# Kernel tuning notes

Measured on AMD Instinct MI355X. Metric: run time of the kernel, lower is better.

The kernel has to match this reference:

```python
import jax, jax.numpy as jnp
import numpy as np

# Static config (matches init_kwargs)
H, G, D = 16, 4, 128          # n_head, n_query_groups, head_size
QPK = H // G                  # queries per kv group = 4
LEFT = 1024 - 1               # sliding-window left width (local_window-1)
SCALE = 1.0 / float(np.sqrt(D))
NEG = jnp.finfo(jnp.float32).min


def _rope(x, cos, sin):
    # x: [B,T,h,D]; cos/sin: [T, D/2]; non-interleaved (flash-attn) convention
    d2 = cos.shape[-1]
    x1, x2 = x[..., :d2], x[..., d2:]
    c = cos[None, :, None, :]
    s = sin[None, :, None, :]
    return jnp.concatenate([x1 * c - x2 * s, x1 * s + x2 * c], axis=-1)


def setup_inputs() -> dict:
    key = jax.random.key(0)
    ks = jax.random.split(key, 4)
    B, T, C = 1, 2048, 2048
    x = jax.random.normal(ks[0], (B, T, C), jnp.float32)
    # real RoPE tables, base 10000
    pos = jnp.arange(T, dtype=jnp.float32)
    inv_freq = 1.0 / (10000.0 ** (jnp.arange(0, D, 2, dtype=jnp.float32) / D))
    ang = pos[:, None] * inv_freq[None, :]        # [T, D/2]
    cos, sin = jnp.cos(ang), jnp.sin(ang)
    W_attn = jax.random.normal(ks[1], ((H + 2 * G) * D, C), jnp.float32) * 0.02
    W_proj = jax.random.normal(ks[2], (C, H * D), jnp.float32) * 0.02
    k_sink = jax.random.normal(ks[3], (G * D,), jnp.float32) * 0.02
    v_sink = jnp.zeros((G * D,), jnp.float32)     # buffer, zeros in original
    return {"x": x, "cos": cos, "sin": sin, "W_attn": W_attn,
            "W_proj": W_proj, "k_sink": k_sink, "v_sink": v_sink}


def reference(x, cos, sin, W_attn, W_proj, k_sink, v_sink):
    B, T, C = x.shape
    # fused QKV projection (no bias)
    qkv = jnp.einsum('btc,oc->bto', x, W_attn)                 # [B,T,(H+2G)*D]
    qkv = qkv.reshape(B, T, G, QPK + 2, D)
    q = qkv[:, :, :, :QPK, :].reshape(B, T, H, D)              # [B,T,H,D]
    k = qkv[:, :, :, QPK, :]                                   # [B,T,G,D]
    v = qkv[:, :, :, QPK + 1, :]                               # [B,T,G,D]
    # RoPE on q and k
    q = _rope(q, cos, sin)
    k = _rope(k, cos, sin)
    # prepend sink token to k/v -> seqlen_k = T+1
    k = jnp.concatenate([jnp.broadcast_to(k_sink.reshape(1, 1, G, D), (B, 1, G, D)), k], axis=1)
    v = jnp.concatenate([jnp.broadcast_to(v_sink.reshape(1, 1, G, D), (B, 1, G, D)), v], axis=1)
    Tk = T + 1
    # GQA: group-major query head layout -> head h uses kv group h // QPK
    kh = jnp.repeat(k, QPK, axis=2)                            # [B,Tk,H,D]
    vh = jnp.repeat(v, QPK, axis=2)
    scores = jnp.einsum('bqhd,bkhd->bhqk', q, kh) * SCALE      # [B,H,T,Tk]
    # flash-attn causal + sliding window, bottom-right aligned: offset = Tk - T
    off = Tk - T
    i = jnp.arange(T)[:, None]
    j = jnp.arange(Tk)[None, :]
    allowed = (j <= i + off) & (j >= i + off - LEFT)
    scores = jnp.where(allowed[None, None], scores, NEG)
    p = jax.nn.softmax(scores, axis=-1)
    o = jnp.einsum('bhqk,bkhd->bqhd', p, vh).reshape(B, T, H * D)
    y = jnp.einsum('btd,cd->btc', o, W_proj)                   # output proj, no bias
    return y
```

## Files before the change

kernel.cpp:

```cpp
#include <hip/hip_runtime.h>

#define T_SEQ  2048
#define TK_SEQ 2049
#define JP     2080
#define SL_F    0.12751744f
#define THR_L2  11.0f

typedef __attribute__((ext_vector_type(8))) short short8;
typedef __attribute__((ext_vector_type(4))) float f32x4;

__device__ __forceinline__ unsigned short f2bf(float f) {
  unsigned int u = __float_as_uint(f);
  u += 0x7fff + ((u >> 16) & 1);
  return (unsigned short)(u >> 16);
}

__device__ __forceinline__ void gload16(const unsigned short* g, unsigned short* l) {
  __builtin_amdgcn_global_load_lds(
      (const __attribute__((address_space(1))) void*)g,
      (__attribute__((address_space(3))) void*)l, 16, 0, 0);
}

__global__ __launch_bounds__(256) void split_pack(const float4* __restrict__ s0,
                                                  unsigned short* __restrict__ d0,
                                                  int n0, int p0,
                                                  const float4* __restrict__ s1,
                                                  unsigned short* __restrict__ d1,
                                                  int n1, int p1) {
  int i = blockIdx.x * 256 + threadIdx.x;
  const float4* s; unsigned short* d; int k, p;
  if (i < n0) { s = s0; d = d0; k = i; p = p0; }
  else { k = i - n0; if (k >= n1) return; s = s1; d = d1; p = p1; }
  float4 f = s[k];
  float fv[4] = {f.x, f.y, f.z, f.w};
  ushort4 hv, lv;
#pragma unroll
  for (int e = 0; e < 4; ++e) {
    unsigned int u = __float_as_uint(fv[e]) & 0xffff0000u;
    ((unsigned short*)&hv)[e] = (unsigned short)(u >> 16);
    ((unsigned short*)&lv)[e] = f2bf(fv[e] - __uint_as_float(u));
  }
  *(ushort4*)(d + 4 * (size_t)k)     = hv;
  *(ushort4*)(d + p + 4 * (size_t)k) = lv;
}

__global__ __launch_bounds__(256, 2) void gemm_sp(const unsigned short* __restrict__ Ag,
                                                  const unsigned short* __restrict__ Bg,
                                                  float* __restrict__ C,
                                                  int M, int N, int K) {
  __shared__ unsigned short Ah[2][128 * 32], Al[2][128 * 32];
  __shared__ unsigned short Bh[2][128 * 32], Bl[2][128 * 32];

  const int tid  = threadIdx.x;
  const int lane = tid & 63;
  const int wid  = tid >> 6;
  const int wm   = (wid >> 1) << 6;
  const int wn   = (wid & 1) << 6;
  const int lo16 = lane & 15;
  const int hi4  = lane >> 4;
  const int m0   = blockIdx.y << 7;
  const int n0   = blockIdx.x << 7;
  const size_t MK = (size_t)M * K;
  const size_t NK = (size_t)N * K;

  const int c0 = (wid << 6) + lane;
  const int c1 = ((4 + wid) << 6) + lane;
  const unsigned short* a0g = Ag + (size_t)(m0 + (c0 >> 2)) * K + ((c0 & 3) << 3);
  const unsigned short* a1g = Ag + (size_t)(m0 + (c1 >> 2)) * K + ((c1 & 3) << 3);
  const unsigned short* b0g = Bg + (size_t)(n0 + (c0 >> 2)) * K + ((c0 & 3) << 3);
  const unsigned short* b1g = Bg + (size_t)(n0 + (c1 >> 2)) * K + ((c1 & 3) << 3);
  const int o0 = wid << 9;
  const int o1 = (4 + wid) << 9;

  int ra[4], rb[4];
#pragma unroll
  for (int i = 0; i < 4; ++i) {
    ra[i] = ((wm + i * 16 + lo16) << 5) + (hi4 << 3);
    rb[i] = ((wn + i * 16 + lo16) << 5) + (hi4 << 3);
  }

  f32x4 acc[4][4];
  const f32x4 z4 = {0.f, 0.f, 0.f, 0.f};
#pragma unroll
  for (int i = 0; i < 4; ++i)
#pragma unroll
    for (int j = 0; j < 4; ++j) acc[i][j] = z4;

  gload16(a0g,      &Ah[0][o0]);
  gload16(a1g,      &Ah[0][o1]);
  gload16(a0g + MK, &Al[0][o0]);
  gload16(a1g + MK, &Al[0][o1]);
  gload16(b0g,      &Bh[0][o0]);
  gload16(b1g,      &Bh[0][o1]);
  gload16(b0g + NK, &Bl[0][o0]);
  gload16(b1g + NK, &Bl[0][o1]);

  int cur = 0;
  for (int k0 = 0; k0 < K; k0 += 32) {
    const bool more = (k0 + 32) < K;
    if (more) {
      const int nxt = cur ^ 1;
      const int kn  = k0 + 32;
      gload16(a0g + kn,      &Ah[nxt][o0]);
      gload16(a1g + kn,      &Ah[nxt][o1]);
      gload16(a0g + MK + kn, &Al[nxt][o0]);
      gload16(a1g + MK + kn, &Al[nxt][o1]);
      gload16(b0g + kn,      &Bh[nxt][o0]);
      gload16(b1g + kn,      &Bh[nxt][o1]);
      gload16(b0g + NK + kn, &Bl[nxt][o0]);
      gload16(b1g + NK + kn, &Bl[nxt][o1]);
      asm volatile("s_waitcnt vmcnt(8)" ::: "memory");
    } else {
      asm volatile("s_waitcnt vmcnt(0)" ::: "memory");
    }
    __builtin_amdgcn_s_barrier();
    __builtin_amdgcn_sched_barrier(0);

    short8 fah[4], fal[4], fbh[4], fbl[4];
#pragma unroll
    for (int i = 0; i < 4; ++i) {
      fah[i] = *(const short8*)&Ah[cur][ra[i]];
      fal[i] = *(const short8*)&Al[cur][ra[i]];
      fbh[i] = *(const short8*)&Bh[cur][rb[i]];
      fbl[i] = *(const short8*)&Bl[cur][rb[i]];
    }
#pragma unroll
    for (int i = 0; i < 4; ++i)
#pragma unroll
      for (int j = 0; j < 4; ++j) {
        acc[i][j] = __builtin_amdgcn_mfma_f32_16x16x32_bf16(fah[i], fbh[j], acc[i][j], 0, 0, 0);
        acc[i][j] = __builtin_amdgcn_mfma_f32_16x16x32_bf16(fal[i], fbh[j], acc[i][j], 0, 0, 0);
        acc[i][j] = __builtin_amdgcn_mfma_f32_16x16x32_bf16(fah[i], fbl[j], acc[i][j], 0, 0, 0);
      }

    __builtin_amdgcn_sched_barrier(0);
    __builtin_amdgcn_s_barrier();
    asm volatile("" ::: "memory");
    cur ^= 1;
  }

#pragma unroll
  for (int i = 0; i < 4; ++i) {
    const int row = m0 + wm + i * 16 + (hi4 << 2);
#pragma unroll
    for (int j = 0; j < 4; ++j) {
      float* cp = C + (size_t)row * N + n0 + wn + j * 16 + lo16;
      cp[0]            = acc[i][j][0];
      cp[(size_t)N]    = acc[i][j][1];
      cp[(size_t)2*N]  = acc[i][j][2];
      cp[(size_t)3*N]  = acc[i][j][3];
    }
  }
}

#define RB_Q  4096
#define RB_K  1024
#define RB_KE 64
#define RB_V  65

__global__ __launch_bounds__(256) void rope2(const float* __restrict__ qkv,
                                             const float* __restrict__ cosb,
                                             const float* __restrict__ sinb,
                                             const float* __restrict__ ksink,
                                             const float* __restrict__ vsink,
                                             unsigned short* __restrict__ qb,
                                             unsigned short* __restrict__ kb,
                                             unsigned short* __restrict__ vtb) {
  __shared__ unsigned short tl[512 * 33];
  const int bid = blockIdx.x, tid = threadIdx.x;
  if (bid < RB_Q) {
    int idx = bid * 256 + tid;
    int t = idx >> 9, rem = idx & 511;
    int h = rem >> 5, dp = (rem & 31) << 1;
    int g = h >> 2, qi = h & 3;
    const float* src = qkv + (size_t)t * 3072 + g * 768 + qi * 128;
    float2 x1 = *(const float2*)(src + dp);
    float2 x2 = *(const float2*)(src + 64 + dp);
    float2 c  = *(const float2*)(cosb + t * 64 + dp);
    float2 s  = *(const float2*)(sinb + t * 64 + dp);
    ushort2 o1 = { f2bf(x1.x * c.x - x2.x * s.x), f2bf(x1.y * c.y - x2.y * s.y) };
    ushort2 o2 = { f2bf(x1.x * s.x + x2.x * c.x), f2bf(x1.y * s.y + x2.y * c.y) };
    *(ushort2*)(qb + (size_t)t * 2048 + h * 128 + dp)      = o1;
    *(ushort2*)(qb + (size_t)t * 2048 + h * 128 + 64 + dp) = o2;
  } else if (bid < RB_Q + RB_K) {
    int idx = (bid - RB_Q) * 256 + tid;
    int t = idx >> 7, rem = idx & 127;
    int g = rem >> 5, dp = (rem & 31) << 1;
    const float* src = qkv + (size_t)t * 3072 + g * 768 + 512;
    float2 x1 = *(const float2*)(src + dp);
    float2 x2 = *(const float2*)(src + 64 + dp);
    float2 c  = *(const float2*)(cosb + t * 64 + dp);
    float2 s  = *(const float2*)(sinb + t * 64 + dp);
    ushort2 o1 = { f2bf(x1.x * c.x - x2.x * s.x), f2bf(x1.y * c.y - x2.y * s.y) };
    ushort2 o2 = { f2bf(x1.x * s.x + x2.x * c.x), f2bf(x1.y * s.y + x2.y * c.y) };
    size_t base = (size_t)(t + 1) * 512 + g * 128 + dp;
    *(ushort2*)(kb + base)      = o1;
    *(ushort2*)(kb + base + 64) = o2;
  } else if (bid < RB_Q + RB_K + RB_KE) {
    int idx = (bid - RB_Q - RB_K) * 256 + tid;
    int jj = idx >> 9, c = idx & 511;
    if (jj == 0) kb[c] = f2bf(ksink[c]);
    else         kb[(size_t)(2048 + jj) * 512 + c] = 0;
  } else {
    int b  = bid - RB_Q - RB_K - RB_KE;
    int j0 = b << 5;
#pragma unroll 4
    for (int st = 0; st < 64; ++st) {
      int id = st * 256 + tid;
      int jj = id >> 9, c = id & 511;
      int j = j0 + jj;
      float val;
      if (j == 0)          val = vsink[c];
      else if (j <= T_SEQ) val = qkv[(size_t)(j - 1) * 3072 + (c >> 7) * 768 + 640 + (c & 127)];
      else                 val = 0.f;
      tl[c * 33 + jj] = f2bf(val);
    }
    __syncthreads();
#pragma unroll 4
    for (int st = 0; st < 32; ++st) {
      int id = st * 256 + tid;
      int row = id >> 4, jp = (id & 15) << 1;
      ushort2 w = { tl[row * 33 + jp], tl[row * 33 + jp + 1] };
      *(ushort2*)(vtb + (size_t)row * JP + j0 + jp) = w;
    }
  }
}

#define KSTR 136
#define VSTR 40

__global__ __launch_bounds__(512) void attn_mfma_bf16(const unsigned short* __restrict__ qb,
                                                      const unsigned short* __restrict__ kb,
                                                      const unsigned short* __restrict__ vtb,
                                                      unsigned short* __restrict__ ofh,
                                                      const float4* __restrict__ wpsrc,
                                                      unsigned short* __restrict__ wps) {
  __shared__ unsigned short Kl[2][32 * KSTR];
  __shared__ unsigned short Vl[2][128 * VSTR];

  const int bid  = blockIdx.x;
  const int tid  = threadIdx.x;
  if (bid >= 256) {
    int k = (bid - 256) * 512 + tid;
    float4 f = wpsrc[k];
    float fv[4] = {f.x, f.y, f.z, f.w};
    ushort4 hv, lv;
#pragma unroll
    for (int e = 0; e < 4; ++e) {
      unsigned int u = __float_as_uint(fv[e]) & 0xffff0000u;
      ((unsigned short*)&hv)[e] = (unsigned short)(u >> 16);
      ((unsigned short*)&lv)[e] = f2bf(fv[e] - __uint_as_float(u));
    }
    *(ushort4*)(wps + 4 * (size_t)k)           = hv;
    *(ushort4*)(wps + 4194304 + 4 * (size_t)k) = lv;
    return;
  }

  const int tile = bid >> 2;
  const int g    = bid & 3;
  const int t0b  = tile << 5;
  const int wv   = tid >> 6;
  const int hq   = wv & 3;
  const int sub  = wv >> 2;
  const int h    = g * 4 + hq;
  const int lane = tid & 63;
  const int lo   = lane & 15;
  const int hi   = lane >> 4;
  const int t0w  = t0b + (sub << 4);
  const int t    = t0w + lo;

  const int sj   = tid >> 4;
  const int sc   = (tid & 15) << 3;
  const int kphi = ((((sj & 7) << 2) | (sj >> 3))) * KSTR + sc;
  const int svd  = tid >> 2;
  const int svj  = (tid & 3) << 3;
  const int vdst = svd * VSTR + svj;
  const unsigned short* ksrc = kb  + (size_t)sj * 512 + g * 128 + sc;
  const unsigned short* vsrc = vtb + (size_t)(g * 128 + svd) * JP + svj;

  short8 qfrag[4];
  {
    const unsigned short* qp = qb + (size_t)t * 2048 + h * 128 + (hi << 3);
#pragma unroll
    for (int d0 = 0; d0 < 4; ++d0) qfrag[d0] = *(const short8*)(qp + d0 * 32);
  }

  f32x4 acc[8];
  const f32x4 z4 = {0.f, 0.f, 0.f, 0.f};
#pragma unroll
  for (int dt = 0; dt < 8; ++dt) acc[dt] = z4;

  float m = -1e4f, l = 0.f;

  int jlo = t0b - 1022; if (jlo < 0) jlo = 0;
  const int jb0  = jlo & ~31;
  const int jmax = t0b + 32;
  const int nch  = ((jmax - jb0) >> 5) + 1;

  const int klA = (((lo & 3) << 2) | (lo >> 2)) * KSTR + (hi << 3);

  uint4 kreg = *(const uint4*)(ksrc + (size_t)jb0 * 512);
  uint4 vreg = *(const uint4*)(vsrc + jb0);
  *(uint4*)&Kl[0][kphi] = kreg;
  *(uint4*)&Vl[0][vdst] = vreg;
  __syncthreads();

  int bsel = 0;
  for (int ci = 0; ci < nch; ++ci) {
    const int jb = jb0 + (ci << 5);
    const bool more = (ci + 1 < nch);
    if (more) {
      const int jn = jb + 32;
      kreg = *(const uint4*)(ksrc + (size_t)jn * 512);
      vreg = *(const uint4*)(vsrc + jn);
    }

    const unsigned short* Kb = &Kl[bsel][0];
    f32x4 sa = z4, sb = z4;
#pragma unroll
    for (int d0 = 0; d0 < 4; ++d0) {
      short8 ka  = *(const short8*)(Kb + klA + d0 * 32);
      short8 kB2 = *(const short8*)(Kb + klA + 16 * KSTR + d0 * 32);
      sa = __builtin_amdgcn_mfma_f32_16x16x32_bf16(ka,  qfrag[d0], sa, 0, 0, 0);
      sb = __builtin_amdgcn_mfma_f32_16x16x32_bf16(kB2, qfrag[d0], sb, 0, 0, 0);
    }

    float z[8];
    const int jbase = jb + (hi << 3);
    const bool interior = (jb >= t0w - 1007) && (jb <= t0w - 30);
    if (interior) {
#pragma unroll
      for (int r = 0; r < 4; ++r) { z[r] = sa[r] * SL_F; z[r + 4] = sb[r] * SL_F; }
    } else {
#pragma unroll
      for (int r = 0; r < 8; ++r) {
        float sv = (r < 4) ? sa[r] : sb[r - 4];
        int j = jbase + r;
        bool valid = (j <= t + 1) && (j >= t - 1022);
        z[r] = valid ? sv * SL_F : -1e30f;
      }
    }

    float lmax = fmaxf(fmaxf(fmaxf(z[0], z[1]), fmaxf(z[2], z[3])),
                       fmaxf(fmaxf(z[4], z[5]), fmaxf(z[6], z[7])));
    if (!__all(lmax <= m + THR_L2)) {
      float cm = lmax;
      cm = fmaxf(cm, __shfl_xor(cm, 16, 64));
      cm = fmaxf(cm, __shfl_xor(cm, 32, 64));
      float mn = fmaxf(m, cm);
      float a  = exp2f(m - mn);
      l *= a;
#pragma unroll
      for (int dt = 0; dt < 8; ++dt) acc[dt] *= a;
      m = mn;
    }

    float p[8];
#pragma unroll
    for (int r = 0; r < 8; ++r) { p[r] = exp2f(z[r] - m); l += p[r]; }

    short8 pfrag;
#pragma unroll
    for (int e = 0; e < 8; ++e) pfrag[e] = (short)f2bf(p[e]);

    const unsigned short* Vb = &Vl[bsel][0];
#pragma unroll
    for (int dt = 0; dt < 8; ++dt) {
      short8 vf = *(const short8*)(Vb + (dt * 16 + lo) * VSTR + (hi << 3));
      acc[dt] = __builtin_amdgcn_mfma_f32_16x16x32_bf16(vf, pfrag, acc[dt], 0, 0, 0);
    }

    if (more) {
      *(uint4*)&Kl[bsel ^ 1][kphi] = kreg;
      *(uint4*)&Vl[bsel ^ 1][vdst] = vreg;
      __syncthreads();
      bsel ^= 1;
    }
  }

  float lt = l;
  lt += __shfl_xor(lt, 16, 64);
  lt += __shfl_xor(lt, 32, 64);
  const float inv = 1.f / lt;

  unsigned short* ofl = ofh + 4194304;
  const size_t elem = (size_t)t * 2048 + h * 128 + (hi << 2);
#pragma unroll
  for (int dt = 0; dt < 8; ++dt) {
    f32x4 o4 = acc[dt] * inv;
    ushort4 hv, lv;
#pragma unroll
    for (int e = 0; e < 4; ++e) {
      unsigned int u = __float_as_uint(o4[e]) & 0xffff0000u;
      ((unsigned short*)&hv)[e] = (unsigned short)(u >> 16);
      ((unsigned short*)&lv)[e] = f2bf(o4[e] - __uint_as_float(u));
    }
    *(ushort4*)(ofh + elem + dt * 16) = hv;
    *(ushort4*)(ofl + elem + dt * 16) = lv;
  }
}

extern "C" void kernel_launch(void* const* d_in, const int* in_sizes, int n_in,
                              void* d_out, int out_size, void* d_ws, size_t ws_size,
                              hipStream_t stream) {
  const float* x     = (const float*)d_in[0];
  const float* cosb  = (const float*)d_in[1];
  const float* sinb  = (const float*)d_in[2];
  const float* Wa    = (const float*)d_in[3];
  const float* Wp    = (const float*)d_in[4];
  const float* ksink = (const float*)d_in[5];
  const float* vsink = (const float*)d_in[6];
  float* y = (float*)d_out;

  char* ws = (char*)d_ws;
  float*          qkv = (float*)ws;
  unsigned short* wps = (unsigned short*)ws;
  unsigned short* was = (unsigned short*)(ws + 25165824);
  unsigned short* ofh = (unsigned short*)(ws + 25165824);
  unsigned short* xs  = (unsigned short*)(ws + 50331648);
  unsigned short* qb  = (unsigned short*)(ws + 50331648);
  unsigned short* kbb = (unsigned short*)(ws + 58720256);
  unsigned short* vtb = (unsigned short*)(ws + 60850176);

  split_pack<<<10240, 256, 0, stream>>>((const float4*)x, xs, 1048576, 4194304,
                                        (const float4*)Wa, was, 1572864, 6291456);
  gemm_sp<<<dim3(24, 16), 256, 0, stream>>>(xs, was, qkv, 2048, 3072, 2048);
  rope2<<<RB_Q + RB_K + RB_KE + RB_V, 256, 0, stream>>>(qkv, cosb, sinb, ksink, vsink,
                                                        qb, kbb, vtb);
  attn_mfma_bf16<<<2304, 512, 0, stream>>>(qb, kbb, vtb, ofh, (const float4*)Wp, wps);
  gemm_sp<<<dim3(16, 16), 256, 0, stream>>>(ofh, wps, y, 2048, 2048, 2048);
}
```

Before: 347.9 us.

## Replace split-bf16 GEMMs with two-limb int8 MFMA GEMMs using per-row scales

Both projection GEMMs now quantize each row to roughly 15-bit fixed point, split into high and low int8 limbs with a per-row scale, and use the 16x16x64 int8 MFMA with three limb products per tile, recombined in the epilogue. This halves operand bytes and uses the int8 matrix path, which publicly has higher peak rate than bf16. The attention output is now written as fp32 and quantized in a separate pass, and the W_proj split-pack is moved out of the attention launch into its own quantization launch. The extra launches and per-row absmax reductions add overhead, and the fixed-point accuracy depends on each row's dynamic range.

```diff
diff --git a/kernel.cpp b/kernel.cpp
--- a/kernel.cpp
+++ b/kernel.cpp
@@ -1,13 +1,13 @@
 #include <hip/hip_runtime.h>
 
 #define T_SEQ  2048
-#define TK_SEQ 2049
 #define JP     2080
 #define SL_F    0.12751744f
 #define THR_L2  11.0f
 
 typedef __attribute__((ext_vector_type(8))) short short8;
 typedef __attribute__((ext_vector_type(4))) float f32x4;
+typedef __attribute__((ext_vector_type(4))) int   i32x4;
 
 __device__ __forceinline__ unsigned short f2bf(float f) {
   unsigned int u = __float_as_uint(f);
@@ -15,41 +15,61 @@
   return (unsigned short)(u >> 16);
 }
 
-__device__ __forceinline__ void gload16(const unsigned short* g, unsigned short* l) {
+__device__ __forceinline__ void gload16(const void* g, void* l) {
   __builtin_amdgcn_global_load_lds(
       (const __attribute__((address_space(1))) void*)g,
       (__attribute__((address_space(3))) void*)l, 16, 0, 0);
 }
 
-__global__ __launch_bounds__(256) void split_pack(const float4* __restrict__ s0,
-                                                  unsigned short* __restrict__ d0,
-                                                  int n0, int p0,
-                                                  const float4* __restrict__ s1,
-                                                  unsigned short* __restrict__ d1,
-                                                  int n1, int p1) {
-  int i = blockIdx.x * 256 + threadIdx.x;
-  const float4* s; unsigned short* d; int k, p;
-  if (i < n0) { s = s0; d = d0; k = i; p = p0; }
-  else { k = i - n0; if (k >= n1) return; s = s1; d = d1; p = p1; }
-  float4 f = s[k];
-  float fv[4] = {f.x, f.y, f.z, f.w};
-  ushort4 hv, lv;
-#pragma unroll
-  for (int e = 0; e < 4; ++e) {
-    unsigned int u = __float_as_uint(fv[e]) & 0xffff0000u;
-    ((unsigned short*)&hv)[e] = (unsigned short)(u >> 16);
-    ((unsigned short*)&lv)[e] = f2bf(fv[e] - __uint_as_float(u));
-  }
-  *(ushort4*)(d + 4 * (size_t)k)     = hv;
-  *(ushort4*)(d + p + 4 * (size_t)k) = lv;
-}
-
-__global__ __launch_bounds__(256, 2) void gemm_sp(const unsigned short* __restrict__ Ag,
-                                                  const unsigned short* __restrict__ Bg,
+__global__ __launch_bounds__(256) void quant_rows(
+    const float* __restrict__ s0, signed char* __restrict__ d0,
+    float* __restrict__ sc0, int n0, int p0,
+    const float* __restrict__ s1, signed char* __restrict__ d1,
+    float* __restrict__ sc1, int n1, int p1) {
+  __shared__ float red[4];
+  int r = blockIdx.x;
+  const float* s; signed char* d; float* sc; int p;
+  if (r < n0) { s = s0; d = d0; sc = sc0; p = p0; }
+  else { r -= n0; if (r >= n1) return; s = s1; d = d1; sc = sc1; p = p1; }
+  const int tid = threadIdx.x;
+  const float4* sp = (const float4*)(s + (size_t)r * 2048) + tid * 2;
+  float4 v0 = sp[0], v1 = sp[1];
+  float vv[8] = {v0.x, v0.y, v0.z, v0.w, v1.x, v1.y, v1.z, v1.w};
+  float am = 0.f;
+#pragma unroll
+  for (int e = 0; e < 8; ++e) am = fmaxf(am, fabsf(vv[e]));
+#pragma unroll
+  for (int o = 1; o <= 32; o <<= 1) am = fmaxf(am, __shfl_xor(am, o, 64));
+  if ((tid & 63) == 0) red[tid >> 6] = am;
+  __syncthreads();
+  am = fmaxf(fmaxf(red[0], red[1]), fmaxf(red[2], red[3]));
+  const float inv = (am > 1e-30f) ? 32512.f / am : 0.f;
+  if (tid == 0) sc[r] = am * (1.f / 32512.f);
+  int hb[8], lb[8];
+#pragma unroll
+  for (int e = 0; e < 8; ++e) {
+    int n  = __float2int_rn(vv[e] * inv);
+    int nh = (n + 128) >> 8;
+    hb[e] = nh & 0xff;
+    lb[e] = (n - (nh << 8)) & 0xff;
+  }
+  int2 hw, lw;
+  hw.x = hb[0] | (hb[1] << 8) | (hb[2] << 16) | (hb[3] << 24);
+  hw.y = hb[4] | (hb[5] << 8) | (hb[6] << 16) | (hb[7] << 24);
+  lw.x = lb[0] | (lb[1] << 8) | (lb[2] << 16) | (lb[3] << 24);
+  lw.y = lb[4] | (lb[5] << 8) | (lb[6] << 16) | (lb[7] << 24);
+  *(int2*)(d + (size_t)r * 2048 + tid * 8)     = hw;
+  *(int2*)(d + p + (size_t)r * 2048 + tid * 8) = lw;
+}
+
+__global__ __launch_bounds__(256, 2) void gemm_i8(const signed char* __restrict__ Ag,
+                                                  const signed char* __restrict__ Bg,
+                                                  const float* __restrict__ sav,
+                                                  const float* __restrict__ sbv,
                                                   float* __restrict__ C,
                                                   int M, int N, int K) {
-  __shared__ unsigned short Ah[2][128 * 32], Al[2][128 * 32];
-  __shared__ unsigned short Bh[2][128 * 32], Bl[2][128 * 32];
+  __shared__ signed char Anh[2][128 * 64], Anl[2][128 * 64];
+  __shared__ signed char Bnh[2][128 * 64], Bnl[2][128 * 64];
 
   const int tid  = threadIdx.x;
   const int lane = tid & 63;
@@ -63,52 +83,53 @@
   const size_t MK = (size_t)M * K;
   const size_t NK = (size_t)N * K;
 
-  const int c0 = (wid << 6) + lane;
-  const int c1 = ((4 + wid) << 6) + lane;
-  const unsigned short* a0g = Ag + (size_t)(m0 + (c0 >> 2)) * K + ((c0 & 3) << 3);
-  const unsigned short* a1g = Ag + (size_t)(m0 + (c1 >> 2)) * K + ((c1 & 3) << 3);
-  const unsigned short* b0g = Bg + (size_t)(n0 + (c0 >> 2)) * K + ((c0 & 3) << 3);
-  const unsigned short* b1g = Bg + (size_t)(n0 + (c1 >> 2)) * K + ((c1 & 3) << 3);
-  const int o0 = wid << 9;
-  const int o1 = (4 + wid) << 9;
+  const int r0 = (wid << 4) + (lane >> 2);
+  const int r1 = r0 + 64;
+  const int cB = (lane & 3) << 4;
+  const signed char* a0g = Ag + (size_t)(m0 + r0) * K + cB;
+  const signed char* a1g = Ag + (size_t)(m0 + r1) * K + cB;
+  const signed char* b0g = Bg + (size_t)(n0 + r0) * K + cB;
+  const signed char* b1g = Bg + (size_t)(n0 + r1) * K + cB;
+  const int o0 = wid << 10;
+  const int o1 = (4 + wid) << 10;
 
   int ra[4], rb[4];
 #pragma unroll
   for (int i = 0; i < 4; ++i) {
-    ra[i] = ((wm + i * 16 + lo16) << 5) + (hi4 << 3);
-    rb[i] = ((wn + i * 16 + lo16) << 5) + (hi4 << 3);
-  }
-
-  f32x4 acc[4][4];
-  const f32x4 z4 = {0.f, 0.f, 0.f, 0.f};
+    ra[i] = ((wm + i * 16 + lo16) << 6) + (hi4 << 4);
+    rb[i] = ((wn + i * 16 + lo16) << 6) + (hi4 << 4);
+  }
+
+  i32x4 acc1[4][4], acc2[4][4];
+  const i32x4 zi = {0, 0, 0, 0};
 #pragma unroll
   for (int i = 0; i < 4; ++i)
 #pragma unroll
-    for (int j = 0; j < 4; ++j) acc[i][j] = z4;
-
-  gload16(a0g,      &Ah[0][o0]);
-  gload16(a1g,      &Ah[0][o1]);
-  gload16(a0g + MK, &Al[0][o0]);
-  gload16(a1g + MK, &Al[0][o1]);
-  gload16(b0g,      &Bh[0][o0]);
-  gload16(b1g,      &Bh[0][o1]);
-  gload16(b0g + NK, &Bl[0][o0]);
-  gload16(b1g + NK, &Bl[0][o1]);
+    for (int j = 0; j < 4; ++j) { acc1[i][j] = zi; acc2[i][j] = zi; }
+
+  gload16(a0g,      &Anh[0][o0]);
+  gload16(a1g,      &Anh[0][o1]);
+  gload16(a0g + MK, &Anl[0][o0]);
+  gload16(a1g + MK, &Anl[0][o1]);
+  gload16(b0g,      &Bnh[0][o0]);
+  gload16(b1g,      &Bnh[0][o1]);
+  gload16(b0g + NK, &Bnl[0][o0]);
+  gload16(b1g + NK, &Bnl[0][o1]);
 
   int cur = 0;
-  for (int k0 = 0; k0 < K; k0 += 32) {
-    const bool more = (k0 + 32) < K;
+  for (int k0 = 0; k0 < K; k0 += 64) {
+    const bool more = (k0 + 64) < K;
     if (more) {
       const int nxt = cur ^ 1;
-      const int kn  = k0 + 32;
-      gload16(a0g + kn,      &Ah[nxt][o0]);
-      gload16(a1g + kn,      &Ah[nxt][o1]);
-      gload16(a0g + MK + kn, &Al[nxt][o0]);
-      gload16(a1g + MK + kn, &Al[nxt][o1]);
-      gload16(b0g + kn,      &Bh[nxt][o0]);
-      gload16(b1g + kn,      &Bh[nxt][o1]);
-      gload16(b0g + NK + kn, &Bl[nxt][o0]);
-      gload16(b1g + NK + kn, &Bl[nxt][o1]);
+      const int kn  = k0 + 64;
+      gload16(a0g + kn,      &Anh[nxt][o0]);
+      gload16(a1g + kn,      &Anh[nxt][o1]);
+      gload16(a0g + MK + kn, &Anl[nxt][o0]);
+      gload16(a1g + MK + kn, &Anl[nxt][o1]);
+      gload16(b0g + kn,      &Bnh[nxt][o0]);
+      gload16(b1g + kn,      &Bnh[nxt][o1]);
+      gload16(b0g + NK + kn, &Bnl[nxt][o0]);
+      gload16(b1g + NK + kn, &Bnl[nxt][o1]);
       asm volatile("s_waitcnt vmcnt(8)" ::: "memory");
     } else {
       asm volatile("s_waitcnt vmcnt(0)" ::: "memory");
@@ -116,21 +137,21 @@
     __builtin_amdgcn_s_barrier();
     __builtin_amdgcn_sched_barrier(0);
 
-    short8 fah[4], fal[4], fbh[4], fbl[4];
+    i32x4 fah[4], fal[4], fbh[4], fbl[4];
 #pragma unroll
     for (int i = 0; i < 4; ++i) {
-      fah[i] = *(const short8*)&Ah[cur][ra[i]];
-      fal[i] = *(const short8*)&Al[cur][ra[i]];
-      fbh[i] = *(const short8*)&Bh[cur][rb[i]];
-      fbl[i] = *(const short8*)&Bl[cur][rb[i]];
+      fah[i] = *(const i32x4*)&Anh[cur][ra[i]];
+      fal[i] = *(const i32x4*)&Anl[cur][ra[i]];
+      fbh[i] = *(const i32x4*)&Bnh[cur][rb[i]];
+      fbl[i] = *(const i32x4*)&Bnl[cur][rb[i]];
     }
 #pragma unroll
     for (int i = 0; i < 4; ++i)
 #pragma unroll
       for (int j = 0; j < 4; ++j) {
-        acc[i][j] = __builtin_amdgcn_mfma_f32_16x16x32_bf16(fah[i], fbh[j], acc[i][j], 0, 0, 0);
-        acc[i][j] = __builtin_amdgcn_mfma_f32_16x16x32_bf16(fal[i], fbh[j], acc[i][j], 0, 0, 0);
-        acc[i][j] = __builtin_amdgcn_mfma_f32_16x16x32_bf16(fah[i], fbl[j], acc[i][j], 0, 0, 0);
+        acc1[i][j] = __builtin_amdgcn_mfma_i32_16x16x64_i8(fah[i], fbh[j], acc1[i][j], 0, 0, 0);
+        acc2[i][j] = __builtin_amdgcn_mfma_i32_16x16x64_i8(fah[i], fbl[j], acc2[i][j], 0, 0, 0);
+        acc2[i][j] = __builtin_amdgcn_mfma_i32_16x16x64_i8(fal[i], fbh[j], acc2[i][j], 0, 0, 0);
       }
 
     __builtin_amdgcn_sched_barrier(0);
@@ -141,14 +162,17 @@
 
 #pragma unroll
   for (int i = 0; i < 4; ++i) {
-    const int row = m0 + wm + i * 16 + (hi4 << 2);
+    const int rowb = m0 + wm + i * 16 + (hi4 << 2);
+    float sa0 = sav[rowb], sa1 = sav[rowb + 1], sa2 = sav[rowb + 2], sa3 = sav[rowb + 3];
 #pragma unroll
     for (int j = 0; j < 4; ++j) {
-      float* cp = C + (size_t)row * N + n0 + wn + j * 16 + lo16;
-      cp[0]            = acc[i][j][0];
-      cp[(size_t)N]    = acc[i][j][1];
-      cp[(size_t)2*N]  = acc[i][j][2];
-      cp[(size_t)3*N]  = acc[i][j][3];
+      const int col = n0 + wn + j * 16 + lo16;
+      const float sb = sbv[col];
+      float* cp = C + (size_t)rowb * N + col;
+      cp[0]           = fmaf(65536.f, (float)acc1[i][j][0], 256.f * (float)acc2[i][j][0]) * sa0 * sb;
+      cp[(size_t)N]   = fmaf(65536.f, (float)acc1[i][j][1], 256.f * (float)acc2[i][j][1]) * sa1 * sb;
+      cp[(size_t)2*N] = fmaf(65536.f, (float)acc1[i][j][2], 256.f * (float)acc2[i][j][2]) * sa2 * sb;
+      cp[(size_t)3*N] = fmaf(65536.f, (float)acc1[i][j][3], 256.f * (float)acc2[i][j][3]) * sa3 * sb;
     }
   }
 }
@@ -232,30 +256,12 @@
 __global__ __launch_bounds__(512) void attn_mfma_bf16(const unsigned short* __restrict__ qb,
                                                       const unsigned short* __restrict__ kb,
                                                       const unsigned short* __restrict__ vtb,
-                                                      unsigned short* __restrict__ ofh,
-                                                      const float4* __restrict__ wpsrc,
-                                                      unsigned short* __restrict__ wps) {
+                                                      float* __restrict__ of) {
   __shared__ unsigned short Kl[2][32 * KSTR];
   __shared__ unsigned short Vl[2][128 * VSTR];
 
   const int bid  = blockIdx.x;
   const int tid  = threadIdx.x;
-  if (bid >= 256) {
-    int k = (bid - 256) * 512 + tid;
-    float4 f = wpsrc[k];
-    float fv[4] = {f.x, f.y, f.z, f.w};
-    ushort4 hv, lv;
-#pragma unroll
-    for (int e = 0; e < 4; ++e) {
-      unsigned int u = __float_as_uint(fv[e]) & 0xffff0000u;
-      ((unsigned short*)&hv)[e] = (unsigned short)(u >> 16);
-      ((unsigned short*)&lv)[e] = f2bf(fv[e] - __uint_as_float(u));
-    }
-    *(ushort4*)(wps + 4 * (size_t)k)           = hv;
-    *(ushort4*)(wps + 4194304 + 4 * (size_t)k) = lv;
-    return;
-  }
-
   const int tile = bid >> 2;
   const int g    = bid & 3;
   const int t0b  = tile << 5;
@@ -383,20 +389,11 @@
   lt += __shfl_xor(lt, 32, 64);
   const float inv = 1.f / lt;
 
-  unsigned short* ofl = ofh + 4194304;
-  const size_t elem = (size_t)t * 2048 + h * 128 + (hi << 2);
+  float* op = of + (size_t)t * 2048 + h * 128 + (hi << 2);
 #pragma unroll
   for (int dt = 0; dt < 8; ++dt) {
     f32x4 o4 = acc[dt] * inv;
-    ushort4 hv, lv;
-#pragma unroll
-    for (int e = 0; e < 4; ++e) {
-      unsigned int u = __float_as_uint(o4[e]) & 0xffff0000u;
-      ((unsigned short*)&hv)[e] = (unsigned short)(u >> 16);
-      ((unsigned short*)&lv)[e] = f2bf(o4[e] - __uint_as_float(u));
-    }
-    *(ushort4*)(ofh + elem + dt * 16) = hv;
-    *(ushort4*)(ofl + elem + dt * 16) = lv;
+    *(f32x4*)(op + dt * 16) = o4;
   }
 }
 
@@ -414,19 +411,28 @@
 
   char* ws = (char*)d_ws;
   float*          qkv = (float*)ws;
-  unsigned short* wps = (unsigned short*)ws;
-  unsigned short* was = (unsigned short*)(ws + 25165824);
-  unsigned short* ofh = (unsigned short*)(ws + 25165824);
-  unsigned short* xs  = (unsigned short*)(ws + 50331648);
-  unsigned short* qb  = (unsigned short*)(ws + 50331648);
-  unsigned short* kbb = (unsigned short*)(ws + 58720256);
-  unsigned short* vtb = (unsigned short*)(ws + 60850176);
-
-  split_pack<<<10240, 256, 0, stream>>>((const float4*)x, xs, 1048576, 4194304,
-                                        (const float4*)Wa, was, 1572864, 6291456);
-  gemm_sp<<<dim3(24, 16), 256, 0, stream>>>(xs, was, qkv, 2048, 3072, 2048);
+  float*          of  = (float*)ws;
+  signed char*    ops = (signed char*)(ws + 16777216);
+  signed char*    was = (signed char*)(ws + 25165824);
+  signed char*    wps = (signed char*)(ws + 25165824);
+  signed char*    xs  = (signed char*)(ws + 38748736);
+  unsigned short* qb  = (unsigned short*)(ws + 38748736);
+  unsigned short* kbb = (unsigned short*)(ws + 47137344);
+  unsigned short* vtb = (unsigned short*)(ws + 49267264);
+  float*          s_x  = (float*)(ws + 51397184);
+  float*          s_wa = (float*)(ws + 51405376);
+  float*          s_wp = (float*)(ws + 51417664);
+  float*          s_o  = (float*)(ws + 51425856);
+
+  quant_rows<<<5120, 256, 0, stream>>>(x, xs, s_x, 2048, 4194304,
+                                       Wa, was, s_wa, 3072, 6291456);
+  gemm_i8<<<dim3(24, 16), 256, 0, stream>>>(xs, was, s_x, s_wa, qkv, 2048, 3072, 2048);
   rope2<<<RB_Q + RB_K + RB_KE + RB_V, 256, 0, stream>>>(qkv, cosb, sinb, ksink, vsink,
                                                         qb, kbb, vtb);
-  attn_mfma_bf16<<<2304, 512, 0, stream>>>(qb, kbb, vtb, ofh, (const float4*)Wp, wps);
-  gemm_sp<<<dim3(16, 16), 256, 0, stream>>>(ofh, wps, y, 2048, 2048, 2048);
-}
+  quant_rows<<<2048, 256, 0, stream>>>(Wp, wps, s_wp, 2048, 4194304,
+                                       Wp, wps, s_wp, 0, 0);
+  attn_mfma_bf16<<<256, 512, 0, stream>>>(qb, kbb, vtb, of);
+  quant_rows<<<2048, 256, 0, stream>>>(of, ops, s_o, 2048, 4194304,
+                                       of, ops, s_o, 0, 0);
+  gemm_i8<<<dim3(16, 16), 256, 0, stream>>>(ops, wps, s_o, s_wp, y, 2048, 2048, 2048);
+}
```

New measurement: 282.2 us. 1.23x faster.
